# Kernel tuning notes

Measured on AMD Instinct MI355X. Metric: run time of the kernel, lower is better.

The kernel has to match this reference:

```python
import jax, jax.numpy as jnp
import numpy as np

GAMMA = 0.99
LAM = 0.95
EPS = 1e-8


def setup_inputs() -> dict:
    key = jax.random.key(0)
    k1, k2, k3 = jax.random.split(key, 3)
    T, N = 2048, 8192
    rewards = jax.random.normal(k1, (T, N), dtype=jnp.float32)
    values = jax.random.normal(k2, (T + 1, N), dtype=jnp.float32)
    dones = jax.random.randint(k3, (T, N), 0, 2, dtype=jnp.int32)
    return {"rewards": rewards, "values": values, "dones": dones}


def reference(rewards, values, dones):
    # rewards: [T, N], values: [T+1, N], dones: [T, N]
    nonterminal = 1.0 - dones.astype(rewards.dtype)        # [T, N]
    # delta_t = r_t + gamma * V_{t+1} * nt_t - V_t
    delta = rewards + GAMMA * values[1:] * nonterminal - values[:-1]
    coef = (GAMMA * LAM) * nonterminal                      # [T, N]

    def step(carry, xs):
        d, c = xs
        a = d + c * carry
        return a, a

    init = jnp.zeros(rewards.shape[1], dtype=rewards.dtype)
    _, advantages = jax.lax.scan(step, init, (delta, coef), reverse=True)
    returns = advantages + values[:-1]
    # torch .std() is unbiased (ddof=1)
    mean = advantages.mean()
    std = advantages.std(ddof=1)
    advantages_norm = (advantages - mean) / (std + EPS)
    return advantages_norm, returns
```

## Files before the change

kernel.cpp:

```cpp
#include <hip/hip_runtime.h>
#include <math.h>

#define GAMMA_ 0.99f
#define GL_ (0.99f * 0.95f)
#define L_ 32

__global__ __launch_bounds__(256)
void gae_pass1(const float* __restrict__ rw, const float* __restrict__ vv,
               const int* __restrict__ dn,
               float* __restrict__ A, float* __restrict__ B,
               float* __restrict__ Sa, float* __restrict__ Sa2,
               float* __restrict__ SaP, float* __restrict__ SP,
               float* __restrict__ SP2, unsigned* __restrict__ mask,
               double* __restrict__ sums,
               int T, int N)
{
    if (blockIdx.x == 0 && blockIdx.y == 0 && threadIdx.x == 0) {
        sums[0] = 0.0; sums[1] = 0.0;
    }
    int n = blockIdx.x * blockDim.x + threadIdx.x;
    int chunk = blockIdx.y;
    if (n >= N) return;
    int s = chunk * L_;
    int e = s + L_; if (e > T) e = T;
    int len = e - s;

    float a = 0.f, P = 1.f;
    float sa = 0.f, sa2 = 0.f, saP = 0.f, sP = 0.f, sP2 = 0.f;
    unsigned mm = 0u;

    if (len == L_) {
        float r[L_], v[L_ + 1];
        int   d[L_];
        #pragma unroll
        for (int k = 0; k < L_; ++k)
            r[k] = rw[(size_t)(s + k) * N + n];
        #pragma unroll
        for (int k = 0; k <= L_; ++k)
            v[k] = vv[(size_t)(s + k) * N + n];
        #pragma unroll
        for (int k = 0; k < L_; ++k)
            d[k] = __builtin_nontemporal_load(&dn[(size_t)(s + k) * N + n]);

        #pragma unroll
        for (int k = L_ - 1; k >= 0; --k) {
            float nt = (d[k] == 0) ? 1.0f : 0.0f;
            float delta = r[k] + GAMMA_ * v[k + 1] * nt - v[k];
            float c = GL_ * nt;
            a = delta + c * a;
            P = c * P;
            sa  += a;
            sa2 += a * a;
            saP += a * P;
            sP  += P;
            sP2 += P * P;
            mm |= (d[k] == 0) ? (1u << k) : 0u;
        }
    } else {
        float vnext = vv[(size_t)e * N + n];
        for (int t = e - 1; t >= s; --t) {
            size_t off = (size_t)t * N + n;
            float r = rw[off];
            int   dd = dn[off];
            float vc = vv[off];
            float nt = (dd == 0) ? 1.0f : 0.0f;
            float delta = r + GAMMA_ * vnext * nt - vc;
            float c = GL_ * nt;
            a = delta + c * a;
            P = c * P;
            sa  += a;
            sa2 += a * a;
            saP += a * P;
            sP  += P;
            sP2 += P * P;
            mm |= (dd == 0) ? (1u << (t - s)) : 0u;
            vnext = vc;
        }
    }

    size_t idx = (size_t)chunk * N + n;
    A[idx]   = a;
    B[idx]   = P;
    Sa[idx]  = sa;
    Sa2[idx] = sa2;
    SaP[idx] = saP;
    SP[idx]  = sP;
    SP2[idx] = sP2;
    mask[idx] = mm;
}

__global__ __launch_bounds__(1024)
void gae_pass2_ws(const float* __restrict__ A, const float* __restrict__ B,
                  const float* __restrict__ Sa, const float* __restrict__ Sa2,
                  const float* __restrict__ SaP, const float* __restrict__ SP,
                  const float* __restrict__ SP2,
                  float* __restrict__ carry, double* __restrict__ sums,
                  int N, int C)
{
    __shared__ double psum[16], psq[16];
    int wid  = threadIdx.x >> 6;
    int lane = threadIdx.x & 63;
    int nwav = blockDim.x >> 6;
    int n = blockIdx.x * nwav + wid;

    float Ah = 0.f, Bh = 1.f;
    float sa = 0.f, sa2 = 0.f, saP = 0.f, sp = 0.f, sp2 = 0.f;
    bool act = (n < N) && (lane < C);
    size_t idx = (size_t)lane * N + n;
    if (act) {
        Ah = A[idx];  Bh = B[idx];
        sa = Sa[idx]; sa2 = Sa2[idx]; saP = SaP[idx];
        sp = SP[idx]; sp2 = SP2[idx];
    }

    #pragma unroll
    for (int d = 1; d < 64; d <<= 1) {
        float Ad = __shfl_down(Ah, d, 64);
        float Bd = __shfl_down(Bh, d, 64);
        if (lane + d < 64) { Ah = fmaf(Bh, Ad, Ah); Bh *= Bd; }
    }
    float e = __shfl_down(Ah, 1, 64);
    if (lane == 63) e = 0.f;

    double lsum = 0.0, lsq = 0.0;
    if (act) {
        carry[idx] = e;
        lsum = (double)(sa + sp * e);
        lsq  = (double)(sa2 + 2.0f * e * saP + (e * e) * sp2);
    }
    for (int off = 32; off > 0; off >>= 1) {
        lsum += __shfl_down(lsum, off, 64);
        lsq  += __shfl_down(lsq, off, 64);
    }
    if (lane == 0) { psum[wid] = lsum; psq[wid] = lsq; }
    __syncthreads();
    if (threadIdx.x == 0) {
        double s = 0.0, s2 = 0.0;
        for (int w = 0; w < nwav; ++w) { s += psum[w]; s2 += psq[w]; }
        atomicAdd(&sums[0], s);
        atomicAdd(&sums[1], s2);
    }
}

__global__ __launch_bounds__(64)
void gae_pass2_seq(const float* __restrict__ A, const float* __restrict__ B,
                   const float* __restrict__ Sa, const float* __restrict__ Sa2,
                   const float* __restrict__ SaP, const float* __restrict__ SP,
                   const float* __restrict__ SP2,
                   float* __restrict__ carry, double* __restrict__ sums,
                   int N, int C)
{
    int n = blockIdx.x * blockDim.x + threadIdx.x;
    double lsum = 0.0, lsq = 0.0;
    if (n < N) {
        float g = 0.f;
        for (int i = C - 1; i >= 0; --i) {
            int idx = i * N + n;
            carry[idx] = g;
            float e = g;
            lsum += (double)(Sa[idx] + SP[idx] * e);
            lsq  += (double)(Sa2[idx] + 2.0f * e * SaP[idx] + (e * e) * SP2[idx]);
            g = A[idx] + B[idx] * g;
        }
    }
    for (int off = 32; off > 0; off >>= 1) {
        lsum += __shfl_down(lsum, off, 64);
        lsq  += __shfl_down(lsq, off, 64);
    }
    if ((threadIdx.x & 63) == 0) {
        atomicAdd(&sums[0], lsum);
        atomicAdd(&sums[1], lsq);
    }
}

__global__ __launch_bounds__(256)
void gae_pass3(const float* __restrict__ rw, const float* __restrict__ vv,
               const unsigned* __restrict__ mask, const float* __restrict__ carry,
               const double* __restrict__ sums,
               float* __restrict__ out_adv, float* __restrict__ out_ret,
               int T, int N, double Minv, double Mm1inv)
{
    int n = blockIdx.x * blockDim.x + threadIdx.x;
    int chunk = blockIdx.y;
    if (n >= N) return;
    int s = chunk * L_;
    int e = s + L_; if (e > T) e = T;
    int len = e - s;

    double S = sums[0], S2 = sums[1];
    float mean = (float)(S * Minv);
    double vard = (S2 - S * S * Minv) * Mm1inv;
    float inv = (float)(1.0 / (sqrt(vard) + 1e-8));

    size_t idx = (size_t)chunk * N + n;
    float a = carry[idx];
    unsigned mm = mask[idx];

    if (len == L_) {
        float r[L_], v[L_ + 1];
        #pragma unroll
        for (int k = 0; k < L_; ++k)
            r[k] = rw[(size_t)(s + k) * N + n];
        #pragma unroll
        for (int k = 0; k <= L_; ++k)
            v[k] = vv[(size_t)(s + k) * N + n];

        #pragma unroll
        for (int k = L_ - 1; k >= 0; --k) {
            float nt = (mm & (1u << k)) ? 1.0f : 0.0f;
            float delta = r[k] + GAMMA_ * v[k + 1] * nt - v[k];
            a = delta + GL_ * nt * a;
            size_t off = (size_t)(s + k) * N + n;
            __builtin_nontemporal_store((a - mean) * inv, &out_adv[off]);
            __builtin_nontemporal_store(a + v[k],        &out_ret[off]);
        }
    } else {
        float vnext = vv[(size_t)e * N + n];
        for (int t = e - 1; t >= s; --t) {
            size_t off = (size_t)t * N + n;
            float r = rw[off];
            float vc = vv[off];
            float nt = (mm & (1u << (t - s))) ? 1.0f : 0.0f;
            float delta = r + GAMMA_ * vnext * nt - vc;
            a = delta + GL_ * nt * a;
            __builtin_nontemporal_store((a - mean) * inv, &out_adv[off]);
            __builtin_nontemporal_store(a + vc,          &out_ret[off]);
            vnext = vc;
        }
    }
}

extern "C" void kernel_launch(void* const* d_in, const int* in_sizes, int n_in,
                              void* d_out, int out_size, void* d_ws, size_t ws_size,
                              hipStream_t stream)
{
    const float* rw = (const float*)d_in[0];
    const float* vv = (const float*)d_in[1];
    const int*   dn = (const int*)d_in[2];

    long long TN = in_sizes[0];
    long long VN = in_sizes[1];
    int N = (int)(VN - TN);
    int T = (int)(TN / N);
    int C = (T + L_ - 1) / L_;

    char* ws = (char*)d_ws;
    double* sums = (double*)ws;
    size_t cn = (size_t)C * N;
    unsigned* mask = (unsigned*)(ws + 16);
    float* f   = (float*)(ws + 16 + cn * 4);
    float* A   = f;
    float* B   = f + cn;
    float* Sa  = f + 2 * cn;
    float* Sa2 = f + 3 * cn;
    float* SaP = f + 4 * cn;
    float* SP  = f + 5 * cn;
    float* SP2 = f + 6 * cn;
    float* cry = f + 7 * cn;

    dim3 blk(256);
    dim3 g1((N + 255) / 256, C);
    gae_pass1<<<g1, blk, 0, stream>>>(
        rw, vv, dn, A, B, Sa, Sa2, SaP, SP, SP2, mask, sums, T, N);

    if (C <= 64) {
        int wpb = 16;
        gae_pass2_ws<<<dim3((N + wpb - 1) / wpb), dim3(wpb * 64), 0, stream>>>(
            A, B, Sa, Sa2, SaP, SP, SP2, cry, sums, N, C);
    } else {
        gae_pass2_seq<<<dim3((N + 63) / 64), dim3(64), 0, stream>>>(
            A, B, Sa, Sa2, SaP, SP, SP2, cry, sums, N, C);
    }

    double M = (double)TN;
    gae_pass3<<<g1, blk, 0, stream>>>(
        rw, vv, mask, cry, sums,
        (float*)d_out, (float*)d_out + TN,
        T, N, 1.0 / M, 1.0 / (M - 1.0));
}
```

Before: 314.7 us.

## Fuse three GAE passes into one cooperative kernel with grid syncs

Adds a single cooperative kernel that runs the chunked scan, the cross-chunk carry scan with the global statistics reduction, and the output pass, separated by grid-wide syncs. The per-thread value chunk and done mask stay in registers across phases, so values and dones are not re-read and the mask buffer is no longer written or read. Chunk length grows to 64. With T=2048 and N=8192 this needs 32*8192/256=1024 blocks resident at once; if the occupancy cap is below that, it falls back to the three-kernel path. The cost is heavy register pressure (65 values kept live) and grid-sync overhead.

```diff
diff --git a/kernel.cpp b/kernel.cpp
--- a/kernel.cpp
+++ b/kernel.cpp
@@ -1,9 +1,133 @@
 #include <hip/hip_runtime.h>
+#include <hip/hip_cooperative_groups.h>
 #include <math.h>
+
+namespace cg = cooperative_groups;
 
 #define GAMMA_ 0.99f
 #define GL_ (0.99f * 0.95f)
 #define L_ 32
+#define LF_ 64
+#define GF_ 16
+
+__global__ __launch_bounds__(256, 4)
+void gae_fused(const float* __restrict__ rw, const float* __restrict__ vv,
+               const int* __restrict__ dn,
+               float* __restrict__ A, float* __restrict__ B,
+               float* __restrict__ Sa, float* __restrict__ Sa2,
+               float* __restrict__ SaP, float* __restrict__ SP,
+               float* __restrict__ SP2, float* __restrict__ carry,
+               double* __restrict__ sums,
+               float* __restrict__ out_adv, float* __restrict__ out_ret,
+               int T, int N, int C2, double Minv, double Mm1inv)
+{
+    int gtid = blockIdx.x * blockDim.x + threadIdx.x;
+    int n = gtid % N;
+    int c = gtid / N;
+    int s = c * LF_;
+    if (gtid == 0) { sums[0] = 0.0; sums[1] = 0.0; }
+
+    float v[LF_ + 1];
+    #pragma unroll
+    for (int k = 0; k <= LF_; ++k)
+        v[k] = vv[(size_t)(s + k) * N + n];
+
+    float a = 0.f, P = 1.f;
+    float sa = 0.f, sa2 = 0.f, saP = 0.f, sP = 0.f, sP2 = 0.f;
+    unsigned long long mm = 0ull;
+
+    #pragma unroll
+    for (int g = LF_ / GF_ - 1; g >= 0; --g) {
+        float r[GF_]; int d[GF_];
+        #pragma unroll
+        for (int i = 0; i < GF_; ++i)
+            r[i] = rw[(size_t)(s + g * GF_ + i) * N + n];
+        #pragma unroll
+        for (int i = 0; i < GF_; ++i)
+            d[i] = __builtin_nontemporal_load(&dn[(size_t)(s + g * GF_ + i) * N + n]);
+        #pragma unroll
+        for (int i = GF_ - 1; i >= 0; --i) {
+            int k = g * GF_ + i;
+            float nt = (d[i] == 0) ? 1.f : 0.f;
+            float delta = r[i] + GAMMA_ * v[k + 1] * nt - v[k];
+            float cc = GL_ * nt;
+            a = delta + cc * a;
+            P = cc * P;
+            sa += a; sa2 += a * a; saP += a * P; sP += P; sP2 += P * P;
+            mm |= (d[i] == 0) ? (1ull << k) : 0ull;
+        }
+    }
+    size_t idx = (size_t)c * N + n;
+    A[idx] = a;  B[idx] = P;
+    Sa[idx] = sa; Sa2[idx] = sa2; SaP[idx] = saP; SP[idx] = sP; SP2[idx] = sP2;
+
+    __threadfence();
+    cg::this_grid().sync();
+
+    {
+        int wglob = blockIdx.x * (blockDim.x >> 6) + (threadIdx.x >> 6);
+        int totw  = gridDim.x * (blockDim.x >> 6);
+        int lane = threadIdx.x & 63, half = lane >> 5, lh = lane & 31;
+        for (int base = wglob * 2; base < N; base += totw * 2) {
+            int col = base + half;
+            bool act = (col < N) && (lh < C2);
+            size_t i2 = (size_t)lh * N + col;
+            float Ah = 0.f, Bh = 1.f;
+            float psa = 0.f, psa2 = 0.f, psaP = 0.f, psP = 0.f, psP2 = 0.f;
+            if (act) {
+                Ah = A[i2]; Bh = B[i2];
+                psa = Sa[i2]; psa2 = Sa2[i2]; psaP = SaP[i2];
+                psP = SP[i2]; psP2 = SP2[i2];
+            }
+            #pragma unroll
+            for (int dd = 1; dd < 32; dd <<= 1) {
+                float Ad = __shfl_down(Ah, dd, 32);
+                float Bd = __shfl_down(Bh, dd, 32);
+                if (lh + dd < 32) { Ah = fmaf(Bh, Ad, Ah); Bh *= Bd; }
+            }
+            float e = __shfl_down(Ah, 1, 32);
+            if (lh == 31) e = 0.f;
+            double lsum = 0.0, lsq = 0.0;
+            if (act) {
+                carry[i2] = e;
+                lsum = (double)(psa + psP * e);
+                lsq  = (double)(psa2 + 2.f * e * psaP + (e * e) * psP2);
+            }
+            for (int off = 32; off > 0; off >>= 1) {
+                lsum += __shfl_down(lsum, off, 64);
+                lsq  += __shfl_down(lsq, off, 64);
+            }
+            if (lane == 0) { atomicAdd(&sums[0], lsum); atomicAdd(&sums[1], lsq); }
+        }
+    }
+
+    __threadfence();
+    cg::this_grid().sync();
+
+    double S = sums[0], S2 = sums[1];
+    float mean = (float)(S * Minv);
+    double vard = (S2 - S * S * Minv) * Mm1inv;
+    float inv = (float)(1.0 / (sqrt(vard) + 1e-8));
+
+    a = carry[idx];
+    #pragma unroll
+    for (int g = LF_ / GF_ - 1; g >= 0; --g) {
+        float r[GF_];
+        #pragma unroll
+        for (int i = 0; i < GF_; ++i)
+            r[i] = rw[(size_t)(s + g * GF_ + i) * N + n];
+        #pragma unroll
+        for (int i = GF_ - 1; i >= 0; --i) {
+            int k = g * GF_ + i;
+            float nt = (mm & (1ull << k)) ? 1.f : 0.f;
+            float delta = r[i] + GAMMA_ * v[k + 1] * nt - v[k];
+            a = delta + GL_ * nt * a;
+            size_t off = (size_t)(s + k) * N + n;
+            __builtin_nontemporal_store((a - mean) * inv, &out_adv[off]);
+            __builtin_nontemporal_store(a + v[k],         &out_ret[off]);
+        }
+    }
+}
 
 __global__ __launch_bounds__(256)
 void gae_pass1(const float* __restrict__ rw, const float* __restrict__ vv,
@@ -49,11 +173,7 @@
             float c = GL_ * nt;
             a = delta + c * a;
             P = c * P;
-            sa  += a;
-            sa2 += a * a;
-            saP += a * P;
-            sP  += P;
-            sP2 += P * P;
+            sa += a; sa2 += a * a; saP += a * P; sP += P; sP2 += P * P;
             mm |= (d[k] == 0) ? (1u << k) : 0u;
         }
     } else {
@@ -68,24 +188,15 @@
             float c = GL_ * nt;
             a = delta + c * a;
             P = c * P;
-            sa  += a;
-            sa2 += a * a;
-            saP += a * P;
-            sP  += P;
-            sP2 += P * P;
+            sa += a; sa2 += a * a; saP += a * P; sP += P; sP2 += P * P;
             mm |= (dd == 0) ? (1u << (t - s)) : 0u;
             vnext = vc;
         }
     }
 
     size_t idx = (size_t)chunk * N + n;
-    A[idx]   = a;
-    B[idx]   = P;
-    Sa[idx]  = sa;
-    Sa2[idx] = sa2;
-    SaP[idx] = saP;
-    SP[idx]  = sP;
-    SP2[idx] = sP2;
+    A[idx] = a;  B[idx] = P;
+    Sa[idx] = sa; Sa2[idx] = sa2; SaP[idx] = saP; SP[idx] = sP; SP2[idx] = sP2;
     mask[idx] = mm;
 }
 
@@ -112,7 +223,6 @@
         sa = Sa[idx]; sa2 = Sa2[idx]; saP = SaP[idx];
         sp = SP[idx]; sp2 = SP2[idx];
     }
-
     #pragma unroll
     for (int d = 1; d < 64; d <<= 1) {
         float Ad = __shfl_down(Ah, d, 64);
@@ -242,10 +352,58 @@
     long long VN = in_sizes[1];
     int N = (int)(VN - TN);
     int T = (int)(TN / N);
-    int C = (T + L_ - 1) / L_;
+    double M = (double)TN;
+    double Minv = 1.0 / M, Mm1inv = 1.0 / (M - 1.0);
+
+    float* out_adv = (float*)d_out;
+    float* out_ret = (float*)d_out + TN;
+
+    int C2 = T / LF_;
+    long long units = (long long)C2 * N;
+    bool fast = (T % LF_ == 0) && (C2 >= 1) && (C2 <= 32) && (units % 256 == 0);
+    int nblk = fast ? (int)(units / 256) : 0;
+
+    static int s_cap = -1;
+    if (fast) {
+        if (s_cap < 0) {
+            int dev = 0; hipGetDevice(&dev);
+            int ncu = 0;
+            hipDeviceGetAttribute(&ncu, hipDeviceAttributeMultiprocessorCount, dev);
+            int perCU = 0;
+            hipOccupancyMaxActiveBlocksPerMultiprocessor(&perCU, gae_fused, 256, 0);
+            s_cap = (ncu > 0 && perCU > 0) ? ncu * perCU : 0;
+        }
+        if (nblk > s_cap) fast = false;
+    }
 
     char* ws = (char*)d_ws;
     double* sums = (double*)ws;
+
+    if (fast) {
+        size_t cn = (size_t)C2 * N;
+        float* f   = (float*)(ws + 16);
+        float* A   = f;
+        float* B   = f + cn;
+        float* Sa  = f + 2 * cn;
+        float* Sa2 = f + 3 * cn;
+        float* SaP = f + 4 * cn;
+        float* SP  = f + 5 * cn;
+        float* SP2 = f + 6 * cn;
+        float* cry = f + 7 * cn;
+
+        void* args[] = {
+            (void*)&rw, (void*)&vv, (void*)&dn,
+            (void*)&A, (void*)&B, (void*)&Sa, (void*)&Sa2, (void*)&SaP,
+            (void*)&SP, (void*)&SP2, (void*)&cry, (void*)&sums,
+            (void*)&out_adv, (void*)&out_ret,
+            (void*)&T, (void*)&N, (void*)&C2, (void*)&Minv, (void*)&Mm1inv
+        };
+        hipError_t err = hipLaunchCooperativeKernel(
+            (void*)gae_fused, dim3(nblk), dim3(256), args, 0, stream);
+        if (err == hipSuccess) return;
+    }
+
+    int C = (T + L_ - 1) / L_;
     size_t cn = (size_t)C * N;
     unsigned* mask = (unsigned*)(ws + 16);
     float* f   = (float*)(ws + 16 + cn * 4);
@@ -272,9 +430,6 @@
             A, B, Sa, Sa2, SaP, SP, SP2, cry, sums, N, C);
     }
 
-    double M = (double)TN;
     gae_pass3<<<g1, blk, 0, stream>>>(
-        rw, vv, mask, cry, sums,
-        (float*)d_out, (float*)d_out + TN,
-        T, N, 1.0 / M, 1.0 / (M - 1.0));
-}
+        rw, vv, mask, cry, sums, out_adv, out_ret, T, N, Minv, Mm1inv);
+}
```

After: 312.3 us. Within noise of the previous version (-0.8%).
